# Kernel optimization log

Measured on AMD Instinct MI355X. Metric: run time of the kernel, lower is better.

## Reference

```python
import jax, jax.numpy as jnp
import numpy as np

GAMMA = 3.0
ALPHA = 1.5
GRID = 32
EPS = 1e-7

N_BOXES = 4_000_000


def _ciou(box1, box2, eps=EPS):
    """Ultralytics bbox_iou with xywh=True, CIoU=True. Returns shape (N,)."""
    x1, y1, w1, h1 = box1[..., 0], box1[..., 1], box1[..., 2], box1[..., 3]
    x2, y2, w2, h2 = box2[..., 0], box2[..., 1], box2[..., 2], box2[..., 3]
    # xywh -> xyxy
    b1x1, b1x2 = x1 - w1 * 0.5, x1 + w1 * 0.5
    b1y1, b1y2 = y1 - h1 * 0.5, y1 + h1 * 0.5
    b2x1, b2x2 = x2 - w2 * 0.5, x2 + w2 * 0.5
    b2y1, b2y2 = y2 - h2 * 0.5, y2 + h2 * 0.5
    # intersection
    iw = jnp.clip(jnp.minimum(b1x2, b2x2) - jnp.maximum(b1x1, b2x1), 0.0, None)
    ih = jnp.clip(jnp.minimum(b1y2, b2y2) - jnp.maximum(b1y1, b2y1), 0.0, None)
    inter = iw * ih
    union = w1 * h1 + w2 * h2 - inter + eps
    iou = inter / union
    # enclosing box diagonal and center distance
    cw = jnp.maximum(b1x2, b2x2) - jnp.minimum(b1x1, b2x1)
    ch = jnp.maximum(b1y2, b2y2) - jnp.minimum(b1y1, b2y1)
    c2 = cw * cw + ch * ch + eps
    rho2 = ((b2x1 + b2x2 - b1x1 - b1x2) ** 2 + (b2y1 + b2y2 - b1y1 - b1y2) ** 2) * 0.25
    # aspect-ratio term; alpha is computed under no_grad in torch -> stop_gradient
    v = (4.0 / (jnp.pi ** 2)) * (jnp.arctan(w2 / h2) - jnp.arctan(w1 / h1)) ** 2
    a = jax.lax.stop_gradient(v / (v - iou + (1.0 + eps)))
    return iou - (rho2 / c2 + v * a)


def _density_map(boxes, grid_size=GRID):
    # scatter-add histogram over box centers (equivalent of the Python for-loop)
    gx = jnp.clip((boxes[..., 0] * grid_size).astype(jnp.int32), 0, grid_size - 1)
    gy = jnp.clip((boxes[..., 1] * grid_size).astype(jnp.int32), 0, grid_size - 1)
    density = jnp.zeros((grid_size, grid_size), boxes.dtype).at[gy, gx].add(1.0)
    return density / jnp.max(density)


def setup_inputs() -> dict:
    key = jax.random.key(0)
    k1, k2 = jax.random.split(key)
    pred_boxes = jax.random.uniform(k1, (N_BOXES, 4), dtype=jnp.float32)
    target_boxes = jax.random.uniform(k2, (N_BOXES, 4), dtype=jnp.float32)
    return {"pred_boxes": pred_boxes, "target_boxes": target_boxes}


def reference(pred_boxes, target_boxes):
    iou = _ciou(pred_boxes, target_boxes)                      # (N,)
    target_areas = target_boxes[..., 2] * target_boxes[..., 3]
    scale_weight = 1.0 / (target_areas + 1e-7)                 # (N,)
    base = (1.0 - iou) ** GAMMA * scale_weight                 # (N,)
    density = _density_map(target_boxes)                       # (32,32)
    density_weight = 1.0 + ALPHA * density                     # (32,32)
    # original: mean over the (1,32,32,N) outer-product broadcast, which
    # factorizes exactly as mean(base) * mean(density_weight)
    return jnp.mean(base) * jnp.mean(density_weight)
```

## Files before the change

kernel.cpp:

```cpp
#include <hip/hip_runtime.h>
#include <math.h>


#define NPART 256
#define GRID_BINS 1024

constexpr float EPSF = 1e-7f;

__global__ __launch_bounds__(1024) void dosa_main(
    const float4* __restrict__ pred, const float4* __restrict__ tgt, int n,
    unsigned* __restrict__ partHist, double* __restrict__ partSum)
{
    __shared__ unsigned lhist[GRID_BINS];
    __shared__ double sdsum[1024];
    for (int i = threadIdx.x; i < GRID_BINS; i += blockDim.x) lhist[i] = 0u;
    __syncthreads();

    float fsum = 0.0f;
    const int stride = gridDim.x * blockDim.x;
    for (int i = blockIdx.x * blockDim.x + threadIdx.x; i < n; i += stride) {
        float4 p = pred[i];
        float4 t = tgt[i];
        float x1 = p.x, y1 = p.y, w1 = p.z, h1 = p.w;
        float x2 = t.x, y2 = t.y, w2 = t.z, h2 = t.w;
        float b1x1 = x1 - w1 * 0.5f, b1x2 = x1 + w1 * 0.5f;
        float b1y1 = y1 - h1 * 0.5f, b1y2 = y1 + h1 * 0.5f;
        float b2x1 = x2 - w2 * 0.5f, b2x2 = x2 + w2 * 0.5f;
        float b2y1 = y2 - h2 * 0.5f, b2y2 = y2 + h2 * 0.5f;
        float iw = fminf(b1x2, b2x2) - fmaxf(b1x1, b2x1); iw = fmaxf(iw, 0.0f);
        float ih = fminf(b1y2, b2y2) - fmaxf(b1y1, b2y1); ih = fmaxf(ih, 0.0f);
        float inter = iw * ih;
        float uni = w1 * h1 + w2 * h2 - inter + EPSF;
        float iou = inter / uni;
        float cw = fmaxf(b1x2, b2x2) - fminf(b1x1, b2x1);
        float ch = fmaxf(b1y2, b2y2) - fminf(b1y1, b2y1);
        float c2 = cw * cw + ch * ch + EPSF;
        float ddx = b2x1 + b2x2 - b1x1 - b1x2;
        float ddy = b2y1 + b2y2 - b1y1 - b1y2;
        float rho2 = (ddx * ddx + ddy * ddy) * 0.25f;
        float dv = atanf(w2 / h2) - atanf(w1 / h1);
        float v = 0.4052847345693511f * (dv * dv);
        float a = v / (v - iou + (1.0f + EPSF));
        float ciou = iou - (rho2 / c2 + v * a);
        float om = 1.0f - ciou;
        float base = om * om * om / (w2 * h2 + 1e-7f);
        fsum += base;
        int gx = (int)(x2 * 32.0f); gx = min(max(gx, 0), 31);
        int gy = (int)(y2 * 32.0f); gy = min(max(gy, 0), 31);
        atomicAdd(&lhist[gy * 32 + gx], 1u);
    }
    __syncthreads();
    for (int i = threadIdx.x; i < GRID_BINS; i += blockDim.x)
        partHist[(size_t)blockIdx.x * GRID_BINS + i] = lhist[i];
    sdsum[threadIdx.x] = (double)fsum;
    __syncthreads();
    for (int off = 512; off > 0; off >>= 1) {
        if (threadIdx.x < off) sdsum[threadIdx.x] += sdsum[threadIdx.x + off];
        __syncthreads();
    }
    if (threadIdx.x == 0) partSum[blockIdx.x] = sdsum[0];
}

__global__ __launch_bounds__(NPART) void dosa_hist_reduce(
    const unsigned* __restrict__ partHist, unsigned* __restrict__ finalHist)
{
    __shared__ unsigned s[NPART];
    int bin = blockIdx.x;
    s[threadIdx.x] = partHist[(size_t)threadIdx.x * GRID_BINS + bin];
    __syncthreads();
    for (int off = NPART / 2; off > 0; off >>= 1) {
        if (threadIdx.x < off) s[threadIdx.x] += s[threadIdx.x + off];
        __syncthreads();
    }
    if (threadIdx.x == 0) finalHist[bin] = s[0];
}

__global__ __launch_bounds__(1024) void dosa_final(
    const unsigned* __restrict__ finalHist, const double* __restrict__ partSum,
    float* __restrict__ out, int n)
{
    __shared__ unsigned sm[1024];
    __shared__ double sd[1024];
    int t = threadIdx.x;
    sm[t] = finalHist[t];
    sd[t] = (t < NPART) ? partSum[t] : 0.0;
    __syncthreads();
    for (int off = 512; off > 0; off >>= 1) {
        if (t < off) {
            sm[t] = max(sm[t], sm[t + off]);
            sd[t] += sd[t + off];
        }
        __syncthreads();
    }
    if (t == 0) {
        double meanBase = sd[0] / (double)n;
        double meanW = 1.0 + 1.5 * ((double)n / (double)sm[0]) / 1024.0;
        out[0] = (float)(meanBase * meanW);
    }
}

extern "C" void kernel_launch(void* const* d_in, const int* in_sizes, int n_in,
                              void* d_out, int out_size, void* d_ws, size_t ws_size,
                              hipStream_t stream) {
    const float4* pred = (const float4*)d_in[0];
    const float4* tgt  = (const float4*)d_in[1];
    int n = in_sizes[0] / 4;

    unsigned* partHist = (unsigned*)d_ws;
    double*   partSum  = (double*)((char*)d_ws + (size_t)NPART * GRID_BINS * 4);
    unsigned* finalHist = (unsigned*)((char*)d_ws + (size_t)NPART * GRID_BINS * 4 + NPART * 8);
    float* out = (float*)d_out;

    dosa_main<<<NPART, 1024, 0, stream>>>(pred, tgt, n, partHist, partSum);
    dosa_hist_reduce<<<GRID_BINS, NPART, 0, stream>>>(partHist, finalHist);
    dosa_final<<<1, 1024, 0, stream>>>(finalHist, partSum, out, n);
}
```

Before: 34.24 us.

## Use fast atan/rcp math, global atomics for histogram, and retune grid

Replaces the two atanf calls with a single polynomial atan of a combined ratio, and swaps divisions for hardware reciprocal approximations. Drops the separate histogram-reduce kernel: each block atomically adds its nonzero local bins into a memset-zeroed global histogram. The grid becomes 2048 blocks of 256 threads, each thread processing two elements per iteration, with a wavefront shuffle reduction replacing the shared-memory tree. The approximate math trades some precision for fewer instructions, and the extra memset launch plus global atomic contention add their own cost.

```diff
diff --git a/kernel.cpp b/kernel.cpp
--- a/kernel.cpp
+++ b/kernel.cpp
@@ -2,77 +2,98 @@
 #include <math.h>
 
 
-#define NPART 256
+#define NBLK 2048
+#define BLOCK 256
 #define GRID_BINS 1024
 
-constexpr float EPSF = 1e-7f;
+__device__ __forceinline__ float rcpf(float x) { return __builtin_amdgcn_rcpf(x); }
 
-__global__ __launch_bounds__(1024) void dosa_main(
+__device__ __forceinline__ float fast_atan(float x) {
+    float ax = fabsf(x);
+    bool big = ax > 1.0f;
+    float t = big ? rcpf(ax) : ax;
+    float s = t * t;
+    float p = -0.0117212f;
+    p = __builtin_fmaf(p, s, 0.05265332f);
+    p = __builtin_fmaf(p, s, -0.11643287f);
+    p = __builtin_fmaf(p, s, 0.19354346f);
+    p = __builtin_fmaf(p, s, -0.33262347f);
+    p = __builtin_fmaf(p, s, 0.99997726f);
+    float r = t * p;
+    r = big ? 1.57079632679f - r : r;
+    return copysignf(r, x);
+}
+
+__device__ __forceinline__ float ciou_base(float4 p, float4 t, unsigned* lhist) {
+    float x1 = p.x, y1 = p.y, w1 = p.z, h1 = p.w;
+    float x2 = t.x, y2 = t.y, w2 = t.z, h2 = t.w;
+    float b1x1 = x1 - w1 * 0.5f, b1x2 = x1 + w1 * 0.5f;
+    float b1y1 = y1 - h1 * 0.5f, b1y2 = y1 + h1 * 0.5f;
+    float b2x1 = x2 - w2 * 0.5f, b2x2 = x2 + w2 * 0.5f;
+    float b2y1 = y2 - h2 * 0.5f, b2y2 = y2 + h2 * 0.5f;
+    float iw = fmaxf(fminf(b1x2, b2x2) - fmaxf(b1x1, b2x1), 0.0f);
+    float ih = fmaxf(fminf(b1y2, b2y2) - fmaxf(b1y1, b2y1), 0.0f);
+    float inter = iw * ih;
+    float uni = w1 * h1 + w2 * h2 - inter + 1e-7f;
+    float iou = inter * rcpf(uni);
+    float cw = fmaxf(b1x2, b2x2) - fminf(b1x1, b2x1);
+    float ch = fmaxf(b1y2, b2y2) - fminf(b1y1, b2y1);
+    float c2 = cw * cw + ch * ch + 1e-7f;
+    float ddx = b2x1 + b2x2 - b1x1 - b1x2;
+    float ddy = b2y1 + b2y2 - b1y1 - b1y2;
+    float rho2 = (ddx * ddx + ddy * ddy) * 0.25f;
+    float dv = fast_atan((w2 * h1 - w1 * h2) * rcpf(h1 * h2 + w1 * w2));
+    float v = 0.4052847345693511f * (dv * dv);
+    float a = v * rcpf(v - iou + (1.0f + 1e-7f));
+    float ciou = iou - (rho2 * rcpf(c2) + v * a);
+    float om = 1.0f - ciou;
+    int gx = min(max((int)(x2 * 32.0f), 0), 31);
+    int gy = min(max((int)(y2 * 32.0f), 0), 31);
+    atomicAdd(&lhist[gy * 32 + gx], 1u);
+    return om * om * om * rcpf(w2 * h2 + 1e-7f);
+}
+
+__global__ __launch_bounds__(BLOCK, 8) void dosa_main(
     const float4* __restrict__ pred, const float4* __restrict__ tgt, int n,
-    unsigned* __restrict__ partHist, double* __restrict__ partSum)
+    unsigned* __restrict__ finalHist, double* __restrict__ partSum)
 {
     __shared__ unsigned lhist[GRID_BINS];
-    __shared__ double sdsum[1024];
-    for (int i = threadIdx.x; i < GRID_BINS; i += blockDim.x) lhist[i] = 0u;
+    __shared__ double wsum[BLOCK / 64];
+    for (int i = threadIdx.x; i < GRID_BINS; i += BLOCK) lhist[i] = 0u;
     __syncthreads();
 
+    const int T = NBLK * BLOCK;
+    int i = blockIdx.x * BLOCK + threadIdx.x;
     float fsum = 0.0f;
-    const int stride = gridDim.x * blockDim.x;
-    for (int i = blockIdx.x * blockDim.x + threadIdx.x; i < n; i += stride) {
-        float4 p = pred[i];
-        float4 t = tgt[i];
-        float x1 = p.x, y1 = p.y, w1 = p.z, h1 = p.w;
-        float x2 = t.x, y2 = t.y, w2 = t.z, h2 = t.w;
-        float b1x1 = x1 - w1 * 0.5f, b1x2 = x1 + w1 * 0.5f;
-        float b1y1 = y1 - h1 * 0.5f, b1y2 = y1 + h1 * 0.5f;
-        float b2x1 = x2 - w2 * 0.5f, b2x2 = x2 + w2 * 0.5f;
-        float b2y1 = y2 - h2 * 0.5f, b2y2 = y2 + h2 * 0.5f;
-        float iw = fminf(b1x2, b2x2) - fmaxf(b1x1, b2x1); iw = fmaxf(iw, 0.0f);
-        float ih = fminf(b1y2, b2y2) - fmaxf(b1y1, b2y1); ih = fmaxf(ih, 0.0f);
-        float inter = iw * ih;
-        float uni = w1 * h1 + w2 * h2 - inter + EPSF;
-        float iou = inter / uni;
-        float cw = fmaxf(b1x2, b2x2) - fminf(b1x1, b2x1);
-        float ch = fmaxf(b1y2, b2y2) - fminf(b1y1, b2y1);
-        float c2 = cw * cw + ch * ch + EPSF;
-        float ddx = b2x1 + b2x2 - b1x1 - b1x2;
-        float ddy = b2y1 + b2y2 - b1y1 - b1y2;
-        float rho2 = (ddx * ddx + ddy * ddy) * 0.25f;
-        float dv = atanf(w2 / h2) - atanf(w1 / h1);
-        float v = 0.4052847345693511f * (dv * dv);
-        float a = v / (v - iou + (1.0f + EPSF));
-        float ciou = iou - (rho2 / c2 + v * a);
-        float om = 1.0f - ciou;
-        float base = om * om * om / (w2 * h2 + 1e-7f);
-        fsum += base;
-        int gx = (int)(x2 * 32.0f); gx = min(max(gx, 0), 31);
-        int gy = (int)(y2 * 32.0f); gy = min(max(gy, 0), 31);
-        atomicAdd(&lhist[gy * 32 + gx], 1u);
+    for (; i + T < n; i += 2 * T) {
+        float4 p0 = pred[i];
+        float4 t0 = tgt[i];
+        float4 p1 = pred[i + T];
+        float4 t1 = tgt[i + T];
+        fsum += ciou_base(p0, t0, lhist);
+        fsum += ciou_base(p1, t1, lhist);
     }
+    if (i < n) {
+        float4 p0 = pred[i];
+        float4 t0 = tgt[i];
+        fsum += ciou_base(p0, t0, lhist);
+    }
+
+    for (int off = 32; off > 0; off >>= 1)
+        fsum += __shfl_down(fsum, off, 64);
+    int lane = threadIdx.x & 63;
+    int wid = threadIdx.x >> 6;
+    if (lane == 0) wsum[wid] = (double)fsum;
     __syncthreads();
-    for (int i = threadIdx.x; i < GRID_BINS; i += blockDim.x)
-        partHist[(size_t)blockIdx.x * GRID_BINS + i] = lhist[i];
-    sdsum[threadIdx.x] = (double)fsum;
-    __syncthreads();
-    for (int off = 512; off > 0; off >>= 1) {
-        if (threadIdx.x < off) sdsum[threadIdx.x] += sdsum[threadIdx.x + off];
-        __syncthreads();
+    for (int b = threadIdx.x; b < GRID_BINS; b += BLOCK) {
+        unsigned c = lhist[b];
+        if (c) atomicAdd(&finalHist[b], c);
     }
-    if (threadIdx.x == 0) partSum[blockIdx.x] = sdsum[0];
-}
-
-__global__ __launch_bounds__(NPART) void dosa_hist_reduce(
-    const unsigned* __restrict__ partHist, unsigned* __restrict__ finalHist)
-{
-    __shared__ unsigned s[NPART];
-    int bin = blockIdx.x;
-    s[threadIdx.x] = partHist[(size_t)threadIdx.x * GRID_BINS + bin];
-    __syncthreads();
-    for (int off = NPART / 2; off > 0; off >>= 1) {
-        if (threadIdx.x < off) s[threadIdx.x] += s[threadIdx.x + off];
-        __syncthreads();
+    if (threadIdx.x == 0) {
+        double s = 0.0;
+        for (int w = 0; w < BLOCK / 64; ++w) s += wsum[w];
+        partSum[blockIdx.x] = s;
     }
-    if (threadIdx.x == 0) finalHist[bin] = s[0];
 }
 
 __global__ __launch_bounds__(1024) void dosa_final(
@@ -83,7 +104,7 @@
     __shared__ double sd[1024];
     int t = threadIdx.x;
     sm[t] = finalHist[t];
-    sd[t] = (t < NPART) ? partSum[t] : 0.0;
+    sd[t] = partSum[t] + partSum[t + 1024];
     __syncthreads();
     for (int off = 512; off > 0; off >>= 1) {
         if (t < off) {
@@ -106,12 +127,11 @@
     const float4* tgt  = (const float4*)d_in[1];
     int n = in_sizes[0] / 4;
 
-    unsigned* partHist = (unsigned*)d_ws;
-    double*   partSum  = (double*)((char*)d_ws + (size_t)NPART * GRID_BINS * 4);
-    unsigned* finalHist = (unsigned*)((char*)d_ws + (size_t)NPART * GRID_BINS * 4 + NPART * 8);
+    unsigned* finalHist = (unsigned*)d_ws;
+    double*   partSum   = (double*)((char*)d_ws + 4096);
     float* out = (float*)d_out;
 
-    dosa_main<<<NPART, 1024, 0, stream>>>(pred, tgt, n, partHist, partSum);
-    dosa_hist_reduce<<<GRID_BINS, NPART, 0, stream>>>(partHist, finalHist);
+    hipMemsetAsync(finalHist, 0, GRID_BINS * sizeof(unsigned), stream);
+    dosa_main<<<NBLK, BLOCK, 0, stream>>>(pred, tgt, n, finalHist, partSum);
     dosa_final<<<1, 1024, 0, stream>>>(finalHist, partSum, out, n);
 }
```

After: 65.95 us. 92.6% more time.
